# Performance work log

Measured on AMD Instinct MI355X. Metric: run time of the kernel, lower is better.

The kernel has to match this reference:

```python
import jax, jax.numpy as jnp
import numpy as np

KSIZE = 7
CUBIC_A = -0.5


def cubic_contribution(x, a=CUBIC_A):
    ax = jnp.abs(x)
    ax2 = ax * ax
    ax3 = ax * ax2
    cont_01 = ((a + 2) * ax3 - (a + 3) * ax2 + 1) * (ax <= 1).astype(x.dtype)
    cont_12 = (a * ax3 - 5 * a * ax2 + 8 * a * ax - 4 * a) * jnp.logical_and(ax > 1, ax <= 2).astype(x.dtype)
    return cont_01 + cont_12


def projective_grid(H, W, m, eps_x=0.0, eps_y=0.0):
    # Apply 3x3 homography m to pixel centers (x+eps_x, y+eps_y); returns (2, H*W).
    xs = jnp.arange(W, dtype=jnp.float32) + eps_x
    ys = jnp.arange(H, dtype=jnp.float32) + eps_y
    yy, xx = jnp.meshgrid(ys, xs, indexing='ij')
    xx = xx.ravel()
    yy = yy.ravel()
    X = m[0, 0] * xx + m[0, 1] * yy + m[0, 2]
    Y = m[1, 0] * xx + m[1, 1] * yy + m[1, 2]
    Z = m[2, 0] * xx + m[2, 1] * yy + m[2, 2]
    return jnp.stack((X / Z, Y / Z))


def setup_inputs() -> dict:
    key = jax.random.key(0)
    k1, k2 = jax.random.split(key)
    H = W = 1024
    N = H * W
    # near-identity homography (avoids degenerate perspective divide)
    m_inverse = jnp.eye(3, dtype=jnp.float32) + 0.001 * jax.random.normal(k1, (3, 3), dtype=jnp.float32)
    # source-space sampling positions, in-image range
    grid = jax.random.uniform(k2, (2, N), dtype=jnp.float32) * jnp.array([[W - 1.0], [H - 1.0]], dtype=jnp.float32)
    yi = jnp.arange(N, dtype=jnp.int32)
    return {"m_inverse": m_inverse, "grid": grid, "H": H, "W": W, "yi": yi}


def reference(m_inverse, grid, H, W, yi):
    K = KSIZE
    pad = K // 2
    offset = (K % 2) / 2  # 0.5 for odd kernels

    pos = grid + 1 - offset                      # (2, N)
    pos_frac = pos - jnp.floor(pos)              # (2, N)

    pl = projective_grid(H, W, m_inverse, eps_x=-0.5)
    pr = projective_grid(H, W, m_inverse, eps_x=0.5)
    pt = projective_grid(H, W, m_inverse, eps_y=-0.5)
    pb = projective_grid(H, W, m_inverse, eps_y=0.5)

    du = (pb - pt)[:, yi][:, :, None, None]      # (2, N, 1, 1)
    dv = (pr - pl)[:, yi][:, :, None, None]      # (2, N, 1, 1)

    # regularize |du| >= 1
    len_du = jnp.sqrt(du[0] ** 2 + du[1] ** 2)   # (N, 1, 1)
    mask_du = len_du < 1.0
    du = jnp.where(mask_du[None], du / len_du[None], du)
    len_du = jnp.where(mask_du, 1.0, len_du)

    # regularize |dv| >= 1
    len_dv = jnp.sqrt(dv[0] ** 2 + dv[1] ** 2)
    mask_dv = len_dv < 1.0
    dv = jnp.where(mask_dv[None], dv / len_dv[None], dv)
    len_dv = jnp.where(mask_dv, 1.0, len_dv)

    det = du[0] * dv[1] - du[1] * dv[0]          # (N, 1, 1)
    len_du = len_du * det
    len_dv = len_dv * det

    pos_w = jnp.linspace(pad - K + 1, pad, K).astype(jnp.float32) + offset  # (K,)
    pw = pos_frac[:, :, None] - pos_w[None, None, :]                        # (2, N, K)
    pos_wx = pw[0][:, None, :]                   # (N, 1, K)
    pos_wy = pw[1][:, :, None]                   # (N, K, 1)

    pos_wxp = (dv[1] * pos_wx - du[1] * pos_wy) / len_du  # (N, K, K)
    pos_wyp = (du[0] * pos_wy - dv[0] * pos_wx) / len_dv  # (N, K, K)

    x = du[0] * pos_wxp + du[1] * pos_wyp        # (N, K, K)
    y = dv[0] * pos_wxp + dv[1] * pos_wyp        # (N, K, K)

    weight = (cubic_contribution(x) * cubic_contribution(y)).reshape(x.shape[0], -1)  # (N, K*K)
    weight = weight / jnp.sum(weight, axis=-1, keepdims=True)
    return weight
```

## Files before the change

kernel.cpp:

```cpp
#include <hip/hip_runtime.h>

#define KK 49
#define BLK 256
#define PPW 32
#define PPB 128
#define WFL (PPW * KK)
#define WF4 (WFL / 4)

static __device__ __forceinline__ float cubicH(float x) {
    const float t  = __builtin_fminf(__builtin_fabsf(x), 2.0f);
    const bool  s  = t < 1.0f;
    const float c3 = s ?  1.5f : -0.5f;
    const float c2 = s ? -2.5f :  2.5f;
    const float c1 = s ?  0.0f : -4.0f;
    const float c0 = s ?  1.0f :  2.0f;
    return __builtin_fmaf(__builtin_fmaf(__builtin_fmaf(c3, t, c2), t, c1), t, c0);
}

__global__ __launch_bounds__(BLK, 6) void kest_kernel(
    const float* __restrict__ m,
    const float* __restrict__ grid,
    const int*   __restrict__ Wp,
    const int*   __restrict__ yi,
    float*       __restrict__ out,
    int N)
{
    __shared__ __align__(16) float lds[4 * WFL];

    const int tid   = threadIdx.x;
    const int wv_   = tid >> 6;
    const int lane  = tid & 63;
    const int pixW  = lane >> 1;
    const int sub   = lane & 1;
    const int blockBase = blockIdx.x * PPB;
    float* ldsW = &lds[wv_ * WFL];

    float Axx = 0.f, Axy = 0.f, Ayx = 0.f, Ayy = 0.f, fxc = 0.f, fyc = 0.f;
    if (lane < 32) {
        const int p = blockBase + wv_ * PPW + lane;
        if (p < N) {
            const float m00 = m[0], m01 = m[1], m02 = m[2];
            const float m10 = m[3], m11 = m[4], m12 = m[5];
            const float m20 = m[6], m21 = m[7], m22 = m[8];
            const int   W   = Wp[0];

            const int j = yi[p];
            int yyI, xxI;
            if ((W & (W - 1)) == 0) {
                yyI = j >> (__ffs(W) - 1);
                xxI = j & (W - 1);
            } else {
                yyI = j / W;
                xxI = j - yyI * W;
            }
            const float xx = (float)xxI, yy = (float)yyI;

            const float X0 = m00 * xx + m01 * yy + m02;
            const float Y0 = m10 * xx + m11 * yy + m12;
            const float Z0 = m20 * xx + m21 * yy + m22;

            const float izy = __builtin_amdgcn_rcpf(Z0 * Z0 - 0.25f * m21 * m21);
            float du0 = (m01 * Z0 - m21 * X0) * izy;
            float du1 = (m11 * Z0 - m21 * Y0) * izy;
            const float izx = __builtin_amdgcn_rcpf(Z0 * Z0 - 0.25f * m20 * m20);
            float dv0 = (m00 * Z0 - m20 * X0) * izx;
            float dv1 = (m10 * Z0 - m20 * Y0) * izx;

            const float d2u = du0 * du0 + du1 * du1;
            const float rlu = __builtin_amdgcn_rsqf(d2u);
            float len_du = d2u * rlu;
            if (len_du < 1.0f) { du0 *= rlu; du1 *= rlu; len_du = 1.0f; }
            const float d2v = dv0 * dv0 + dv1 * dv1;
            const float rlv = __builtin_amdgcn_rsqf(d2v);
            float len_dv = d2v * rlv;
            if (len_dv < 1.0f) { dv0 *= rlv; dv1 *= rlv; len_dv = 1.0f; }

            const float det  = du0 * dv1 - du1 * dv0;
            const float r_du = __builtin_amdgcn_rcpf(len_du * det);
            const float r_dv = __builtin_amdgcn_rcpf(len_dv * det);

            const float p1 = du0 * dv1, p2 = du1 * dv0;
            Axx = p1 * r_du - p2 * r_dv;
            Axy = du0 * du1 * (r_dv - r_du);
            Ayx = dv0 * dv1 * (r_du - r_dv);
            Ayy = p1 * r_dv - p2 * r_du;

            const float px = grid[p]     + 0.5f;
            const float py = grid[N + p] + 0.5f;
            fxc = (px - __builtin_floorf(px)) + 2.5f;
            fyc = (py - __builtin_floorf(py)) + 2.5f;
        }
    }
    Axx = __shfl(Axx, pixW); Axy = __shfl(Axy, pixW);
    Ayx = __shfl(Ayx, pixW); Ayy = __shfl(Ayy, pixW);
    fxc = __shfl(fxc, pixW); fyc = __shfl(fyc, pixW);

    const int i = blockBase + wv_ * PPW + pixW;
    if (i < N) {
        const float subf = (float)sub;

        const float fx1 = fxc - subf;
        const float fx6 = __builtin_fmaf(6.0f, subf, fxc);
        const float fy1 = fyc - subf;

        float w0[13], w1[13];
        float ws = 0.0f;
#pragma unroll
        for (int j = 0; j < 13; ++j) {
            {
                const int qb  = 4 * j;
                const int cxb = qb % 7,            ryb = qb / 7;
                const int dx  = (qb + 1) % 7 - cxb;
                const int dy  = (qb + 1) / 7 - ryb;
                const float wx = (dx == 1 ? fx1 : fx6) - (float)cxb;
                const float wy = (dy == 0 ? fyc : fy1) - (float)ryb;
                const float x_ = __builtin_fmaf(Axx, wx, Axy * wy);
                const float y_ = __builtin_fmaf(Ayx, wx, Ayy * wy);
                float w = cubicH(x_) * cubicH(y_);
                if (j == 12) w *= (1.0f - subf);
                w0[j] = w;
                ws += w;
            }
            if (j < 12) {
                const int qb  = 4 * j + 2;
                const int cxb = qb % 7,            ryb = qb / 7;
                const int dx  = (qb + 1) % 7 - cxb;
                const int dy  = (qb + 1) / 7 - ryb;
                const float wx = (dx == 1 ? fx1 : fx6) - (float)cxb;
                const float wy = (dy == 0 ? fyc : fy1) - (float)ryb;
                const float x_ = __builtin_fmaf(Axx, wx, Axy * wy);
                const float y_ = __builtin_fmaf(Ayx, wx, Ayy * wy);
                const float w = cubicH(x_) * cubicH(y_);
                w1[j] = w;
                ws += w;
            } else {
                w1[j] = 0.0f;
            }
        }
        float wsum = ws + __shfl_xor(ws, 1);
        const float rs = __builtin_amdgcn_rcpf(wsum);

        float* base = &ldsW[pixW * KK + sub];
#pragma unroll
        for (int j = 0; j < 13; ++j) {
            if (j < 12) {
                base[4 * j]     = w0[j] * rs;
                base[4 * j + 2] = w1[j] * rs;
            } else if (sub == 0) {
                base[48] = w0[12] * rs;
            }
        }
    }

    const long long dstF4 = (long long)blockIdx.x * (PPB * KK / 4) + wv_ * WF4;
    if (blockBase + PPB <= N) {
        const float4* src = (const float4*)ldsW;
        float4* dst = (float4*)out + dstF4;
#pragma unroll
        for (int k = 0; k < 7; ++k) {
            const int t = lane + 64 * k;
            if (t < WF4) dst[t] = src[t];
        }
    } else {
        const float* s = (const float*)ldsW;
        const long long baseF = dstF4 * 4;
        const long long limF  = (long long)N * KK;
        for (int t = lane; t < WFL; t += 64)
            if (baseF + t < limF) out[baseF + t] = s[t];
    }
}

extern "C" void kernel_launch(void* const* d_in, const int* in_sizes, int n_in,
                              void* d_out, int out_size, void* d_ws, size_t ws_size,
                              hipStream_t stream) {
    const float* m    = (const float*)d_in[0];
    const float* grid = (const float*)d_in[1];
    const int*   Wp   = (const int*)d_in[3];
    const int*   yi   = (const int*)d_in[4];
    float*       out  = (float*)d_out;
    const int N = in_sizes[4];

    const int blocks = (N + PPB - 1) / PPB;
    kest_kernel<<<blocks, BLK, 0, stream>>>(m, grid, Wp, yi, out, N);
}
```

Before: 219.8 us.

## Split each pixel's 49 weights across four lanes and drop shuffle broadcast

Each pixel's 7x7 weight computation is now spread over four lanes instead of two, so a wave handles 16 pixels and a block 64. Every lane computes the per-pixel homography parameters redundantly instead of broadcasting them via shuffles from 32 lanes. Per-lane register arrays shrink and the launch bound targets more resident waves, aiming at higher occupancy and shorter per-thread work. In exchange, the homography math is repeated four times per pixel and there are twice as many blocks, each with smaller stores.

New measurement: 234.5 us. 1.07x slower.

```diff
diff --git a/kernel.cpp b/kernel.cpp
--- a/kernel.cpp
+++ b/kernel.cpp
@@ -2,8 +2,8 @@
 
 #define KK 49
 #define BLK 256
-#define PPW 32
-#define PPB 128
+#define PPW 16
+#define PPB 64
 #define WFL (PPW * KK)
 #define WF4 (WFL / 4)
 
@@ -17,7 +17,7 @@
     return __builtin_fmaf(__builtin_fmaf(__builtin_fmaf(c3, t, c2), t, c1), t, c0);
 }
 
-__global__ __launch_bounds__(BLK, 6) void kest_kernel(
+__global__ __launch_bounds__(BLK, 8) void kest_kernel(
     const float* __restrict__ m,
     const float* __restrict__ grid,
     const int*   __restrict__ Wp,
@@ -30,124 +30,100 @@
     const int tid   = threadIdx.x;
     const int wv_   = tid >> 6;
     const int lane  = tid & 63;
-    const int pixW  = lane >> 1;
-    const int sub   = lane & 1;
+    const int pixW  = lane >> 2;
+    const int sub   = lane & 3;
     const int blockBase = blockIdx.x * PPB;
     float* ldsW = &lds[wv_ * WFL];
 
-    float Axx = 0.f, Axy = 0.f, Ayx = 0.f, Ayy = 0.f, fxc = 0.f, fyc = 0.f;
-    if (lane < 32) {
-        const int p = blockBase + wv_ * PPW + lane;
-        if (p < N) {
-            const float m00 = m[0], m01 = m[1], m02 = m[2];
-            const float m10 = m[3], m11 = m[4], m12 = m[5];
-            const float m20 = m[6], m21 = m[7], m22 = m[8];
-            const int   W   = Wp[0];
+    const int i = blockBase + wv_ * PPW + pixW;
 
-            const int j = yi[p];
-            int yyI, xxI;
-            if ((W & (W - 1)) == 0) {
-                yyI = j >> (__ffs(W) - 1);
-                xxI = j & (W - 1);
-            } else {
-                yyI = j / W;
-                xxI = j - yyI * W;
-            }
-            const float xx = (float)xxI, yy = (float)yyI;
+    if (i < N) {
+        const float m00 = m[0], m01 = m[1], m02 = m[2];
+        const float m10 = m[3], m11 = m[4], m12 = m[5];
+        const float m20 = m[6], m21 = m[7], m22 = m[8];
+        const int   W   = Wp[0];
 
-            const float X0 = m00 * xx + m01 * yy + m02;
-            const float Y0 = m10 * xx + m11 * yy + m12;
-            const float Z0 = m20 * xx + m21 * yy + m22;
+        const int j = yi[i];
+        int yyI, xxI;
+        if ((W & (W - 1)) == 0) {
+            yyI = j >> (__ffs(W) - 1);
+            xxI = j & (W - 1);
+        } else {
+            yyI = j / W;
+            xxI = j - yyI * W;
+        }
+        const float xx = (float)xxI, yy = (float)yyI;
 
-            const float izy = __builtin_amdgcn_rcpf(Z0 * Z0 - 0.25f * m21 * m21);
-            float du0 = (m01 * Z0 - m21 * X0) * izy;
-            float du1 = (m11 * Z0 - m21 * Y0) * izy;
-            const float izx = __builtin_amdgcn_rcpf(Z0 * Z0 - 0.25f * m20 * m20);
-            float dv0 = (m00 * Z0 - m20 * X0) * izx;
-            float dv1 = (m10 * Z0 - m20 * Y0) * izx;
+        const float X0 = m00 * xx + m01 * yy + m02;
+        const float Y0 = m10 * xx + m11 * yy + m12;
+        const float Z0 = m20 * xx + m21 * yy + m22;
 
-            const float d2u = du0 * du0 + du1 * du1;
-            const float rlu = __builtin_amdgcn_rsqf(d2u);
-            float len_du = d2u * rlu;
-            if (len_du < 1.0f) { du0 *= rlu; du1 *= rlu; len_du = 1.0f; }
-            const float d2v = dv0 * dv0 + dv1 * dv1;
-            const float rlv = __builtin_amdgcn_rsqf(d2v);
-            float len_dv = d2v * rlv;
-            if (len_dv < 1.0f) { dv0 *= rlv; dv1 *= rlv; len_dv = 1.0f; }
+        const float izy = __builtin_amdgcn_rcpf(Z0 * Z0 - 0.25f * m21 * m21);
+        float du0 = (m01 * Z0 - m21 * X0) * izy;
+        float du1 = (m11 * Z0 - m21 * Y0) * izy;
+        const float izx = __builtin_amdgcn_rcpf(Z0 * Z0 - 0.25f * m20 * m20);
+        float dv0 = (m00 * Z0 - m20 * X0) * izx;
+        float dv1 = (m10 * Z0 - m20 * Y0) * izx;
 
-            const float det  = du0 * dv1 - du1 * dv0;
-            const float r_du = __builtin_amdgcn_rcpf(len_du * det);
-            const float r_dv = __builtin_amdgcn_rcpf(len_dv * det);
+        const float d2u = du0 * du0 + du1 * du1;
+        const float rlu = __builtin_amdgcn_rsqf(d2u);
+        float len_du = d2u * rlu;
+        if (len_du < 1.0f) { du0 *= rlu; du1 *= rlu; len_du = 1.0f; }
+        const float d2v = dv0 * dv0 + dv1 * dv1;
+        const float rlv = __builtin_amdgcn_rsqf(d2v);
+        float len_dv = d2v * rlv;
+        if (len_dv < 1.0f) { dv0 *= rlv; dv1 *= rlv; len_dv = 1.0f; }
 
-            const float p1 = du0 * dv1, p2 = du1 * dv0;
-            Axx = p1 * r_du - p2 * r_dv;
-            Axy = du0 * du1 * (r_dv - r_du);
-            Ayx = dv0 * dv1 * (r_du - r_dv);
-            Ayy = p1 * r_dv - p2 * r_du;
+        const float det  = du0 * dv1 - du1 * dv0;
+        const float r_du = __builtin_amdgcn_rcpf(len_du * det);
+        const float r_dv = __builtin_amdgcn_rcpf(len_dv * det);
 
-            const float px = grid[p]     + 0.5f;
-            const float py = grid[N + p] + 0.5f;
-            fxc = (px - __builtin_floorf(px)) + 2.5f;
-            fyc = (py - __builtin_floorf(py)) + 2.5f;
-        }
-    }
-    Axx = __shfl(Axx, pixW); Axy = __shfl(Axy, pixW);
-    Ayx = __shfl(Ayx, pixW); Ayy = __shfl(Ayy, pixW);
-    fxc = __shfl(fxc, pixW); fyc = __shfl(fyc, pixW);
+        const float p1 = du0 * dv1, p2 = du1 * dv0;
+        const float Axx = p1 * r_du - p2 * r_dv;
+        const float Axy = du0 * du1 * (r_dv - r_du);
+        const float Ayx = dv0 * dv1 * (r_du - r_dv);
+        const float Ayy = p1 * r_dv - p2 * r_du;
 
-    const int i = blockBase + wv_ * PPW + pixW;
-    if (i < N) {
-        const float subf = (float)sub;
+        const float px = grid[i]     + 0.5f;
+        const float py = grid[N + i] + 0.5f;
+        const float fxc = (px - __builtin_floorf(px)) + 2.5f;
+        const float fyc = (py - __builtin_floorf(py)) + 2.5f;
 
-        const float fx1 = fxc - subf;
-        const float fx6 = __builtin_fmaf(6.0f, subf, fxc);
-        const float fy1 = fyc - subf;
+        const float g = fxc - (float)sub;
+        float ux[14];
+#pragma unroll
+        for (int k = 0; k < 14; ++k) ux[k] = g - (float)(k - 7);
+        float vy[8];
+#pragma unroll
+        for (int a = 0; a < 8; ++a) vy[a] = fyc - (float)a;
 
-        float w0[13], w1[13];
+        float w[13];
         float ws = 0.0f;
 #pragma unroll
-        for (int j = 0; j < 13; ++j) {
-            {
-                const int qb  = 4 * j;
-                const int cxb = qb % 7,            ryb = qb / 7;
-                const int dx  = (qb + 1) % 7 - cxb;
-                const int dy  = (qb + 1) / 7 - ryb;
-                const float wx = (dx == 1 ? fx1 : fx6) - (float)cxb;
-                const float wy = (dy == 0 ? fyc : fy1) - (float)ryb;
-                const float x_ = __builtin_fmaf(Axx, wx, Axy * wy);
-                const float y_ = __builtin_fmaf(Ayx, wx, Ayy * wy);
-                float w = cubicH(x_) * cubicH(y_);
-                if (j == 12) w *= (1.0f - subf);
-                w0[j] = w;
-                ws += w;
-            }
-            if (j < 12) {
-                const int qb  = 4 * j + 2;
-                const int cxb = qb % 7,            ryb = qb / 7;
-                const int dx  = (qb + 1) % 7 - cxb;
-                const int dy  = (qb + 1) / 7 - ryb;
-                const float wx = (dx == 1 ? fx1 : fx6) - (float)cxb;
-                const float wy = (dy == 0 ? fyc : fy1) - (float)ryb;
-                const float x_ = __builtin_fmaf(Axx, wx, Axy * wy);
-                const float y_ = __builtin_fmaf(Ayx, wx, Ayy * wy);
-                const float w = cubicH(x_) * cubicH(y_);
-                w1[j] = w;
-                ws += w;
-            } else {
-                w1[j] = 0.0f;
-            }
+        for (int jj = 0; jj < 13; ++jj) {
+            const int qb = 4 * jj;
+            const int c  = qb % 7, a = qb / 7;
+            const bool cond = (sub >= 7 - c);
+            const float wx = cond ? ux[c]     : ux[c + 7];
+            const float wy = cond ? vy[a + 1] : vy[a];
+            const float x_ = __builtin_fmaf(Axx, wx, Axy * wy);
+            const float y_ = __builtin_fmaf(Ayx, wx, Ayy * wy);
+            float wt = cubicH(x_) * cubicH(y_);
+            if (jj == 12) wt = (sub == 0) ? wt : 0.0f;
+            w[jj] = wt;
+            ws += wt;
         }
-        float wsum = ws + __shfl_xor(ws, 1);
-        const float rs = __builtin_amdgcn_rcpf(wsum);
+        ws += __shfl_xor(ws, 1);
+        ws += __shfl_xor(ws, 2);
+        const float rs = __builtin_amdgcn_rcpf(ws);
 
         float* base = &ldsW[pixW * KK + sub];
 #pragma unroll
-        for (int j = 0; j < 13; ++j) {
-            if (j < 12) {
-                base[4 * j]     = w0[j] * rs;
-                base[4 * j + 2] = w1[j] * rs;
+        for (int jj = 0; jj < 13; ++jj) {
+            if (jj < 12) {
+                base[4 * jj] = w[jj] * rs;
             } else if (sub == 0) {
-                base[48] = w0[12] * rs;
+                base[48] = w[12] * rs;
             }
         }
     }
@@ -157,7 +133,7 @@
         const float4* src = (const float4*)ldsW;
         float4* dst = (float4*)out + dstF4;
 #pragma unroll
-        for (int k = 0; k < 7; ++k) {
+        for (int k = 0; k < 4; ++k) {
             const int t = lane + 64 * k;
             if (t < WF4) dst[t] = src[t];
         }
```
